# Kernel tuning notes

Hardware: AMD Instinct MI355X
Metric: run time of the kernel (lower is better)

## Reference

```python
import jax, jax.numpy as jnp
import numpy as np

B, L = 8, 2500
VOCAB = 50000 + 2
E = 100          # dims[0], embed size
D = 128          # dims[1], conv filters
Y = 8921         # number of ICD9 labels
K = 9            # conv kernel size
PAD = K // 2


def setup_inputs() -> dict:
    key = jax.random.key(0)
    ks = jax.random.split(key, 8)
    x = jax.random.randint(ks[0], (B, L), 0, 50000)                      # token ids
    target = jax.random.uniform(ks[1], (B, Y), dtype=jnp.float32)        # soft binary targets
    emb_table = jax.random.normal(ks[2], (VOCAB, E), dtype=jnp.float32) * 0.1
    emb_table = emb_table.at[0].set(0.0)                                 # padding_idx=0
    # xavier-uniform-ish scales
    conv_w = jax.random.uniform(ks[3], (D, E, K), dtype=jnp.float32,
                                minval=-1.0, maxval=1.0) * np.sqrt(6.0 / (E * K + D * K))
    conv_b = jnp.zeros((D,), dtype=jnp.float32)
    U = jax.random.uniform(ks[4], (Y, D), dtype=jnp.float32,
                           minval=-1.0, maxval=1.0) * np.sqrt(6.0 / (Y + D))
    final_w = jax.random.uniform(ks[5], (Y, D), dtype=jnp.float32,
                                 minval=-1.0, maxval=1.0) * np.sqrt(6.0 / (Y + D))
    final_b = jnp.zeros((Y,), dtype=jnp.float32)
    return {"x": x, "target": target, "emb_table": emb_table,
            "conv_w": conv_w, "conv_b": conv_b, "U": U,
            "final_w": final_w, "final_b": final_b}


def _bce_with_logits(logits, target):
    # mean(max(z,0) - z*t + log(1+exp(-|z|)))
    return jnp.mean(jnp.maximum(logits, 0.0) - logits * target
                    + jnp.log1p(jnp.exp(-jnp.abs(logits))))


def reference(x, target, emb_table, conv_w, conv_b, U, final_w, final_b):
    e = emb_table[x]                                  # [B, L, E]  (dropout inactive at eval)
    # Conv1d over sequence, 'same' padding; conv_w is torch layout (Cout, Cin, K)
    h = jax.lax.conv_general_dilated(
        e, conv_w, window_strides=(1,), padding=[(PAD, PAD)],
        dimension_numbers=("NWC", "OIW", "NWC")) + conv_b
    h = jnp.tanh(h)                                   # [B, L, D]
    # Label-wise attention: scores [B, Y, L], softmax over sequence dim
    scores = jnp.einsum("yd,bld->byl", U, h)
    alpha = jax.nn.softmax(scores, axis=2)            # [B, Y, L]
    m = jnp.einsum("byl,bld->byd", alpha, h)          # [B, Y, D]
    logits = jnp.einsum("yd,byd->by", final_w, m) + final_b   # [B, Y]
    loss = _bce_with_logits(logits, target)
    yhat = jax.nn.sigmoid(logits)
    return yhat, loss, alpha
```

## Files before the change

### kernel.cpp

```cpp
#include <hip/hip_runtime.h>
#include <math.h>

#define B 8
#define LSEQ 2500
#define EDIM 100
#define DDIM 128
#define YLAB 8921
#define KW 9
#define BYTOT (B*YLAB)
#define LP 2560
#define NLBS 20
#define NYB 70
#define NPB 140

typedef __attribute__((ext_vector_type(8))) short bf16x8;
typedef __attribute__((ext_vector_type(8))) unsigned short u16x8;
typedef __attribute__((ext_vector_type(4))) float f32x4;

__device__ __forceinline__ ushort f2bf(float f){
    union { float f; unsigned u; } v; v.f = f;
    unsigned r = v.u + 0x7FFFu + ((v.u >> 16) & 1u);
    return (ushort)(r >> 16);
}
__device__ __forceinline__ float bf2f(ushort u){
    union { unsigned u; float f; } v; v.u = ((unsigned)u) << 16;
    return v.f;
}

#define OFF_HB 0
#define OFF_HT 1310720
#define OFF_UB 2621440
#define OFF_PS 3192384
#define OFF_LG 4691112
#define OFF_LSP 4762480
#define OFF_WT 4762608

#define NP1 (DDIM*EDIM*KW)
#define NP2 (YLAB*DDIM)
#define NP3 (B*DDIM*(LP-LSEQ))
#define NP4 (B*(LP-LSEQ)*DDIM)
__global__ __launch_bounds__(256) void k_prep(const float* __restrict__ w, const float* __restrict__ U,
                                              float* __restrict__ wT, ushort* __restrict__ Ub,
                                              ushort* __restrict__ hT, ushort* __restrict__ hb){
    int i = blockIdx.x * 256 + threadIdx.x;
    if (i < NP1) {
        int k = i % KW, e = (i / KW) % EDIM, d = i / (KW * EDIM);
        wT[(k * EDIM + e) * DDIM + d] = w[i];
    }
    int i2 = i - NP1;
    if (i2 >= 0 && i2 < NP2) Ub[i2] = f2bf(U[i2]);
    int i3 = i - NP1 - NP2;
    if (i3 >= 0 && i3 < NP3) {
        int c = i3 % (LP - LSEQ), bd = i3 / (LP - LSEQ);
        hT[(size_t)bd * LP + LSEQ + c] = 0;
    }
    int i4 = i - NP1 - NP2 - NP3;
    if (i4 >= 0 && i4 < NP4) {
        int b = i4 / ((LP - LSEQ) * DDIM);
        int r = i4 % ((LP - LSEQ) * DDIM);
        int l = LSEQ + r / DDIM, d = r % DDIM;
        hb[((size_t)b * LP + l) * DDIM + d] = 0;
    }
}

#define CTL 20
__global__ __launch_bounds__(256) void k_conv(const int* __restrict__ x, const float* __restrict__ emb,
                                              const float* __restrict__ wT, const float* __restrict__ bias,
                                              ushort* __restrict__ hb, ushort* __restrict__ hT) {
    __shared__ float se[EDIM * 32];
    __shared__ ushort hstage[DDIM][CTL + 2];
    int blk = blockIdx.x;
    int b = blk / (LSEQ / CTL);
    int l0 = (blk % (LSEQ / CTL)) * CTL;
    int tid = threadIdx.x;
    for (int i = tid; i < (CTL + 8) * EDIM; i += 256) {
        int row = i / EDIM, e = i - row * EDIM;
        int l = l0 + row - 4;
        float v = 0.f;
        if (l >= 0 && l < LSEQ) {
            int tok = x[b * LSEQ + l];
            v = emb[(size_t)tok * EDIM + e];
        }
        se[e * 32 + row] = v;
    }
    __syncthreads();
    int d = tid & 127;
    int g = tid >> 7;
    float bv = bias[d];
    float acc[10];
#pragma unroll
    for (int li = 0; li < 10; li++) acc[li] = bv;
    for (int e = 0; e < EDIM; e++) {
        float r[20];
#pragma unroll
        for (int t2 = 0; t2 < 10; t2++) {
            float2 rr = *(const float2*)&se[e * 32 + g * 10 + 2 * t2];
            r[2 * t2] = rr.x; r[2 * t2 + 1] = rr.y;
        }
#pragma unroll
        for (int k = 0; k < KW; k++) {
            float wv = wT[(k * EDIM + e) * DDIM + d];
#pragma unroll
            for (int li = 0; li < 10; li++) acc[li] += r[li + k] * wv;
        }
    }
#pragma unroll
    for (int li = 0; li < 10; li++) {
        int l = l0 + g * 10 + li;
        ushort u = f2bf(tanhf(acc[li]));
        hb[((size_t)b * LP + l) * DDIM + d] = u;
        hstage[d][g * 10 + li] = u;
    }
    __syncthreads();
    int d2 = tid >> 1, half = tid & 1;
    size_t base = ((size_t)b * DDIM + d2) * LP + l0 + half * 10;
#pragma unroll
    for (int q = 0; q < 10; q++) hT[base + q] = hstage[d2][half * 10 + q];
}

__global__ __launch_bounds__(256) void k_sums(const ushort* __restrict__ hb, const ushort* __restrict__ Ub,
                                              float* __restrict__ psum) {
    int wg = blockIdx.x;
    int b = wg & 7;
    int r = wg >> 3;
    int lblk = r % NLBS, yblk = r / NLBS;
    int l0 = lblk * 128, y0 = yblk * 128;
    int tid = threadIdx.x, w = tid >> 6, lane = tid & 63, g = lane >> 4, ln = lane & 15;
    int y0w = y0 + w * 32;
    bf16x8 zf = {0, 0, 0, 0, 0, 0, 0, 0};
    bf16x8 au[2][4];
    bool vya[2];
#pragma unroll
    for (int yg = 0; yg < 2; yg++) {
        int y = y0w + yg * 16 + ln;
        vya[yg] = y < YLAB;
        const ushort* Ap = Ub + (size_t)(vya[yg] ? y : 0) * DDIM + g * 8;
#pragma unroll
        for (int kk = 0; kk < 4; kk++) au[yg][kk] = vya[yg] ? *(const bf16x8*)(Ap + kk * 32) : zf;
    }
    const ushort* hbB = hb + (size_t)b * LP * DDIM;
    f32x4 zero4 = {0.f, 0.f, 0.f, 0.f};
    float ts[2] = {0.f, 0.f};
#pragma unroll
    for (int lt = 0; lt < 4; lt++) {
        int lw = l0 + lt * 32;
        bf16x8 a[2][4];
#pragma unroll
        for (int fl = 0; fl < 2; fl++)
#pragma unroll
            for (int kk = 0; kk < 4; kk++)
                a[fl][kk] = *(const bf16x8*)(hbB + (size_t)(lw + fl * 16 + ln) * DDIM + kk * 32 + g * 8);
        f32x4 sc[2][2];
        sc[0][0] = zero4; sc[0][1] = zero4; sc[1][0] = zero4; sc[1][1] = zero4;
#pragma unroll
        for (int kk = 0; kk < 4; kk++)
#pragma unroll
            for (int fl = 0; fl < 2; fl++) {
                sc[0][fl] = __builtin_amdgcn_mfma_f32_16x16x32_bf16(a[fl][kk], au[0][kk], sc[0][fl], 0, 0, 0);
                sc[1][fl] = __builtin_amdgcn_mfma_f32_16x16x32_bf16(a[fl][kk], au[1][kk], sc[1][fl], 0, 0, 0);
            }
#pragma unroll
        for (int yg = 0; yg < 2; yg++)
#pragma unroll
            for (int fl = 0; fl < 2; fl++) {
                int lb = lw + fl * 16 + g * 4;
#pragma unroll
                for (int j = 0; j < 4; j++)
                    ts[yg] += (lb + j < LSEQ) ? __expf(sc[yg][fl][j]) : 0.f;
            }
    }
#pragma unroll
    for (int yg = 0; yg < 2; yg++) {
        float t = ts[yg];
        t += __shfl_xor(t, 16, 64);
        t += __shfl_xor(t, 32, 64);
        if (g == 0 && vya[yg])
            psum[(size_t)lblk * BYTOT + b * YLAB + y0w + yg * 16 + ln] = t;
    }
}

__global__ __launch_bounds__(256) void k_pool(const ushort* __restrict__ hb, const ushort* __restrict__ hT,
                                              const ushort* __restrict__ Ub, const float* __restrict__ psum,
                                              const float* __restrict__ fw, const float* __restrict__ fb,
                                              float* __restrict__ alpha, float* __restrict__ yhat,
                                              float* __restrict__ logits) {
    __shared__ ushort hbs[32 * 128];
    __shared__ ushort hts[128 * 40];
    __shared__ ushort et[4][16 * 44];
    __shared__ float rinvS[64];
    int wg = blockIdx.x;
    int b = wg & 7;
    int y0 = (wg >> 3) * 64;
    int tid = threadIdx.x, w = tid >> 6, lane = tid & 63, g = lane >> 4, ln = lane & 15;
    int y0w = y0 + w * 16;
    bf16x8 zf = {0, 0, 0, 0, 0, 0, 0, 0};
    int ya = y0w + ln;
    bool vya = ya < YLAB;
    const ushort* Ap = Ub + (size_t)(vya ? ya : 0) * DDIM + g * 8;
    bf16x8 au[4];
#pragma unroll
    for (int kk = 0; kk < 4; kk++) au[kk] = vya ? *(const bf16x8*)(Ap + kk * 32) : zf;
    if (tid < 64) {
        int y = y0 + tid;
        float s = 1.f;
        if (y < YLAB) {
            s = 0.f;
#pragma unroll
            for (int j = 0; j < NLBS; j++) s += psum[(size_t)j * BYTOT + b * YLAB + y];
        }
        rinvS[tid] = 1.f / s;
    }
    f32x4 zero4 = {0.f, 0.f, 0.f, 0.f};
    f32x4 accm[8];
#pragma unroll
    for (int fd = 0; fd < 8; fd++) accm[fd] = zero4;

    int s0 = tid, s1 = tid + 256;
    const ushort* hbB = hb + (size_t)b * LP * DDIM;
    const ushort* htB = hT + (size_t)b * DDIM * LP;
    int l_a = s0 >> 4, sg_a = s0 & 15, l_b = s1 >> 4, sg_b = s1 & 15;
    int d_a = s0 >> 2, q_a = s0 & 3, d_b = s1 >> 2, q_b = s1 & 3;
    int wsg_a = sg_a ^ (l_a & 7), wsg_b = sg_b ^ (l_b & 7);
    u16x8 rhb0, rhb1, rht0, rht1;
    rhb0 = *(const u16x8*)(hbB + (size_t)l_a * DDIM + sg_a * 8);
    rhb1 = *(const u16x8*)(hbB + (size_t)l_b * DDIM + sg_b * 8);
    rht0 = *(const u16x8*)(htB + (size_t)d_a * LP + q_a * 8);
    rht1 = *(const u16x8*)(htB + (size_t)d_b * LP + q_b * 8);

    float* aB = alpha + (size_t)b * YLAB * LSEQ;
    float rvl = 0.f;
    bool first = true;

    for (int l0 = 0; l0 < LP; l0 += 32) {
        *(u16x8*)&hbs[l_a * DDIM + wsg_a * 8] = rhb0;
        *(u16x8*)&hbs[l_b * DDIM + wsg_b * 8] = rhb1;
        *(u16x8*)&hts[d_a * 40 + q_a * 8] = rht0;
        *(u16x8*)&hts[d_b * 40 + q_b * 8] = rht1;
        __syncthreads();
        if (first) { rvl = vya ? rinvS[w * 16 + ln] : 0.f; first = false; }
        if (l0 + 32 < LP) {
            int ln0 = l0 + 32;
            rhb0 = *(const u16x8*)(hbB + (size_t)(ln0 + l_a) * DDIM + sg_a * 8);
            rhb1 = *(const u16x8*)(hbB + (size_t)(ln0 + l_b) * DDIM + sg_b * 8);
            rht0 = *(const u16x8*)(htB + (size_t)d_a * LP + ln0 + q_a * 8);
            rht1 = *(const u16x8*)(htB + (size_t)d_b * LP + ln0 + q_b * 8);
        }
        f32x4 sc[2];
        sc[0] = zero4; sc[1] = zero4;
#pragma unroll
        for (int kk = 0; kk < 4; kk++)
#pragma unroll
            for (int fl = 0; fl < 2; fl++) {
                int lrow = fl * 16 + ln;
                int slotr = (kk * 4 + g) ^ (lrow & 7);
                bf16x8 bv = *(const bf16x8*)&hbs[lrow * DDIM + slotr * 8];
                sc[fl] = __builtin_amdgcn_mfma_f32_16x16x32_bf16(bv, au[kk], sc[fl], 0, 0, 0);
            }
#pragma unroll
        for (int fl = 0; fl < 2; fl++) {
            float an0 = __expf(sc[fl][0]) * rvl;
            float an1 = __expf(sc[fl][1]) * rvl;
            float an2 = __expf(sc[fl][2]) * rvl;
            float an3 = __expf(sc[fl][3]) * rvl;
            unsigned long long pk =
                (unsigned long long)f2bf(an0) | ((unsigned long long)f2bf(an1) << 16) |
                ((unsigned long long)f2bf(an2) << 32) | ((unsigned long long)f2bf(an3) << 48);
            *(unsigned long long*)&et[w][ln * 44 + fl * 16 + g * 4] = pk;
        }
        bf16x8 af = *(const bf16x8*)&et[w][ln * 44 + g * 8];
#pragma unroll
        for (int fd = 0; fd < 8; fd++) {
            bf16x8 bt = *(const bf16x8*)&hts[(fd * 16 + ln) * 40 + g * 8];
            accm[fd] = __builtin_amdgcn_mfma_f32_16x16x32_bf16(af, bt, accm[fd], 0, 0, 0);
        }
        if (l0 + 32 <= LSEQ) {
#pragma unroll
            for (int i = 0; i < 8; i++) {
                int r = i * 2 + (lane >> 5);
                int c = lane & 31;
                int y = y0w + r;
                if (y < YLAB) aB[(size_t)y * LSEQ + l0 + c] = bf2f(et[w][r * 44 + c]);
            }
        } else if (l0 < LSEQ) {
#pragma unroll
            for (int i = 0; i < 8; i++) {
                int r = i * 2 + (lane >> 5);
                int c = lane & 31;
                int y = y0w + r;
                int l = l0 + c;
                if (y < YLAB && l < LSEQ) aB[(size_t)y * LSEQ + l] = bf2f(et[w][r * 44 + c]);
            }
        }
        __syncthreads();
    }
    float lp[4] = {0.f, 0.f, 0.f, 0.f};
#pragma unroll
    for (int j = 0; j < 4; j++) {
        int yr = y0w + g * 4 + j;
        bool vr = yr < YLAB;
#pragma unroll
        for (int fd = 0; fd < 8; fd++) {
            float fwv = vr ? fw[(size_t)yr * DDIM + fd * 16 + ln] : 0.f;
            lp[j] += accm[fd][j] * fwv;
        }
    }
#pragma unroll
    for (int j = 0; j < 4; j++) {
        float t = lp[j];
        t += __shfl_xor(t, 1, 64); t += __shfl_xor(t, 2, 64);
        t += __shfl_xor(t, 4, 64); t += __shfl_xor(t, 8, 64);
        lp[j] = t;
    }
    if (ln == 0) {
#pragma unroll
        for (int j = 0; j < 4; j++) {
            int yr = y0w + g * 4 + j;
            if (yr < YLAB) {
                float lg = lp[j] + fb[yr];
                int idx = b * YLAB + yr;
                logits[idx] = lg;
                yhat[idx] = 1.f / (1.f + expf(-lg));
            }
        }
    }
}

__global__ __launch_bounds__(256) void k_loss1(const float* __restrict__ logits, const float* __restrict__ target,
                                               float* __restrict__ partials) {
    int tid = threadIdx.x;
    int base = blockIdx.x * 1024;
    float sum = 0.f;
#pragma unroll
    for (int q = 0; q < 4; q++) {
        int i = base + q * 256 + tid;
        if (i < BYTOT) {
            float z = logits[i], t = target[i];
            sum += fmaxf(z, 0.f) - z * t + log1pf(expf(-fabsf(z)));
        }
    }
    for (int o = 32; o > 0; o >>= 1) sum += __shfl_down(sum, o, 64);
    __shared__ float red[4];
    if ((tid & 63) == 0) red[tid >> 6] = sum;
    __syncthreads();
    if (tid == 0) partials[blockIdx.x] = red[0] + red[1] + red[2] + red[3];
}

__global__ __launch_bounds__(128) void k_loss2(const float* __restrict__ partials, float* __restrict__ out_loss) {
    int tid = threadIdx.x;
    float s = (tid < 70) ? partials[tid] : 0.f;
    for (int o = 32; o > 0; o >>= 1) s += __shfl_down(s, o, 64);
    __shared__ float red[2];
    if ((tid & 63) == 0) red[tid >> 6] = s;
    __syncthreads();
    if (tid == 0) out_loss[0] = (red[0] + red[1]) / (float)BYTOT;
}

extern "C" void kernel_launch(void* const* d_in, const int* in_sizes, int n_in,
                              void* d_out, int out_size, void* d_ws, size_t ws_size,
                              hipStream_t stream) {
    const int* x = (const int*)d_in[0];
    const float* target = (const float*)d_in[1];
    const float* emb = (const float*)d_in[2];
    const float* conv_w = (const float*)d_in[3];
    const float* conv_b = (const float*)d_in[4];
    const float* U = (const float*)d_in[5];
    const float* fw = (const float*)d_in[6];
    const float* fb = (const float*)d_in[7];

    float* out = (float*)d_out;
    float* yhat = out;
    float* loss = out + BYTOT;
    float* alpha = out + BYTOT + 1;

    float* ws = (float*)d_ws;
    ushort* hb = (ushort*)(ws + OFF_HB);
    ushort* hT = (ushort*)(ws + OFF_HT);
    ushort* Ub = (ushort*)(ws + OFF_UB);
    float* psum = ws + OFF_PS;
    float* logits = ws + OFF_LG;
    float* lpart = ws + OFF_LSP;
    float* wT = ws + OFF_WT;

    k_prep<<<(NP1 + NP2 + NP3 + NP4 + 255) / 256, 256, 0, stream>>>(conv_w, U, wT, Ub, hT, hb);
    k_conv<<<B * (LSEQ / CTL), 256, 0, stream>>>(x, emb, wT, conv_b, hb, hT);
    k_sums<<<NYB * NLBS * B, 256, 0, stream>>>(hb, Ub, psum);
    k_pool<<<NPB * B, 256, 0, stream>>>(hb, hT, Ub, psum, fw, fb, alpha, yhat, logits);
    k_loss1<<<70, 256, 0, stream>>>(logits, target, lpart);
    k_loss2<<<1, 128, 0, stream>>>(lpart, loss);
}
```

Baseline: 664.9 us.

## Load pooling operands directly from global memory, drop LDS staging and block barriers

```diff
diff --git a/kernel.cpp b/kernel.cpp
--- a/kernel.cpp
+++ b/kernel.cpp
@@ -12,9 +12,9 @@
 #define NLBS 20
 #define NYB 70
 #define NPB 140
+#define LPOOL 2528
 
 typedef __attribute__((ext_vector_type(8))) short bf16x8;
-typedef __attribute__((ext_vector_type(8))) unsigned short u16x8;
 typedef __attribute__((ext_vector_type(4))) float f32x4;
 
 __device__ __forceinline__ ushort f2bf(float f){
@@ -184,10 +184,7 @@
                                               const float* __restrict__ fw, const float* __restrict__ fb,
                                               float* __restrict__ alpha, float* __restrict__ yhat,
                                               float* __restrict__ logits) {
-    __shared__ ushort hbs[32 * 128];
-    __shared__ ushort hts[128 * 40];
     __shared__ ushort et[4][16 * 44];
-    __shared__ float rinvS[64];
     int wg = blockIdx.x;
     int b = wg & 7;
     int y0 = (wg >> 3) * 64;
@@ -200,62 +197,36 @@
     bf16x8 au[4];
 #pragma unroll
     for (int kk = 0; kk < 4; kk++) au[kk] = vya ? *(const bf16x8*)(Ap + kk * 32) : zf;
-    if (tid < 64) {
-        int y = y0 + tid;
-        float s = 1.f;
-        if (y < YLAB) {
-            s = 0.f;
-#pragma unroll
-            for (int j = 0; j < NLBS; j++) s += psum[(size_t)j * BYTOT + b * YLAB + y];
-        }
-        rinvS[tid] = 1.f / s;
+    float rvl = 0.f;
+    if (vya) {
+        float s = 0.f;
+#pragma unroll
+        for (int j = 0; j < NLBS; j++) s += psum[(size_t)j * BYTOT + b * YLAB + ya];
+        rvl = 1.f / s;
     }
     f32x4 zero4 = {0.f, 0.f, 0.f, 0.f};
     f32x4 accm[8];
 #pragma unroll
     for (int fd = 0; fd < 8; fd++) accm[fd] = zero4;
 
-    int s0 = tid, s1 = tid + 256;
     const ushort* hbB = hb + (size_t)b * LP * DDIM;
     const ushort* htB = hT + (size_t)b * DDIM * LP;
-    int l_a = s0 >> 4, sg_a = s0 & 15, l_b = s1 >> 4, sg_b = s1 & 15;
-    int d_a = s0 >> 2, q_a = s0 & 3, d_b = s1 >> 2, q_b = s1 & 3;
-    int wsg_a = sg_a ^ (l_a & 7), wsg_b = sg_b ^ (l_b & 7);
-    u16x8 rhb0, rhb1, rht0, rht1;
-    rhb0 = *(const u16x8*)(hbB + (size_t)l_a * DDIM + sg_a * 8);
-    rhb1 = *(const u16x8*)(hbB + (size_t)l_b * DDIM + sg_b * 8);
-    rht0 = *(const u16x8*)(htB + (size_t)d_a * LP + q_a * 8);
-    rht1 = *(const u16x8*)(htB + (size_t)d_b * LP + q_b * 8);
-
     float* aB = alpha + (size_t)b * YLAB * LSEQ;
-    float rvl = 0.f;
-    bool first = true;
-
-    for (int l0 = 0; l0 < LP; l0 += 32) {
-        *(u16x8*)&hbs[l_a * DDIM + wsg_a * 8] = rhb0;
-        *(u16x8*)&hbs[l_b * DDIM + wsg_b * 8] = rhb1;
-        *(u16x8*)&hts[d_a * 40 + q_a * 8] = rht0;
-        *(u16x8*)&hts[d_b * 40 + q_b * 8] = rht1;
-        __syncthreads();
-        if (first) { rvl = vya ? rinvS[w * 16 + ln] : 0.f; first = false; }
-        if (l0 + 32 < LP) {
-            int ln0 = l0 + 32;
-            rhb0 = *(const u16x8*)(hbB + (size_t)(ln0 + l_a) * DDIM + sg_a * 8);
-            rhb1 = *(const u16x8*)(hbB + (size_t)(ln0 + l_b) * DDIM + sg_b * 8);
-            rht0 = *(const u16x8*)(htB + (size_t)d_a * LP + ln0 + q_a * 8);
-            rht1 = *(const u16x8*)(htB + (size_t)d_b * LP + ln0 + q_b * 8);
-        }
+
+    for (int l0 = 0; l0 < LPOOL; l0 += 32) {
+        bf16x8 hbf[2][4];
+#pragma unroll
+        for (int fl = 0; fl < 2; fl++)
+#pragma unroll
+            for (int kk = 0; kk < 4; kk++)
+                hbf[fl][kk] = *(const bf16x8*)(hbB + (size_t)(l0 + fl * 16 + ln) * DDIM + kk * 32 + g * 8);
         f32x4 sc[2];
         sc[0] = zero4; sc[1] = zero4;
 #pragma unroll
         for (int kk = 0; kk < 4; kk++)
 #pragma unroll
-            for (int fl = 0; fl < 2; fl++) {
-                int lrow = fl * 16 + ln;
-                int slotr = (kk * 4 + g) ^ (lrow & 7);
-                bf16x8 bv = *(const bf16x8*)&hbs[lrow * DDIM + slotr * 8];
-                sc[fl] = __builtin_amdgcn_mfma_f32_16x16x32_bf16(bv, au[kk], sc[fl], 0, 0, 0);
-            }
+            for (int fl = 0; fl < 2; fl++)
+                sc[fl] = __builtin_amdgcn_mfma_f32_16x16x32_bf16(hbf[fl][kk], au[kk], sc[fl], 0, 0, 0);
 #pragma unroll
         for (int fl = 0; fl < 2; fl++) {
             float an0 = __expf(sc[fl][0]) * rvl;
@@ -270,7 +241,7 @@
         bf16x8 af = *(const bf16x8*)&et[w][ln * 44 + g * 8];
 #pragma unroll
         for (int fd = 0; fd < 8; fd++) {
-            bf16x8 bt = *(const bf16x8*)&hts[(fd * 16 + ln) * 40 + g * 8];
+            bf16x8 bt = *(const bf16x8*)(htB + (size_t)(fd * 16 + ln) * LP + l0 + g * 8);
             accm[fd] = __builtin_amdgcn_mfma_f32_16x16x32_bf16(af, bt, accm[fd], 0, 0, 0);
         }
         if (l0 + 32 <= LSEQ) {
@@ -291,7 +262,6 @@
                 if (y < YLAB && l < LSEQ) aB[(size_t)y * LSEQ + l] = bf2f(et[w][r * 44 + c]);
             }
         }
-        __syncthreads();
     }
     float lp[4] = {0.f, 0.f, 0.f, 0.f};
 #pragma unroll
```

After: 1.034 ms. 1.56x slower.
